# Kernel tuning notes

Measured on AMD Instinct MI355X. Metric: run time of the kernel, lower is better.

## Reference

```python
import jax, jax.numpy as jnp
import numpy as np

B, SIZE_IN, SIZE_OUT = 64, 1024, 1024


def setup_inputs() -> dict:
    key = jax.random.key(0)
    ks = jax.random.split(key, 6)
    mu_in = jax.random.normal(ks[0], (B, SIZE_IN), jnp.float32)
    # PSD input covariance: low-rank + jitter (sigma_in is a covariance matrix)
    L = jax.random.normal(ks[1], (B, SIZE_IN, 16), jnp.float32)
    sigma_in = jnp.einsum('bik,bjk->bij', L, L) / 16.0 + 1e-3 * jnp.eye(SIZE_IN, dtype=jnp.float32)
    bound = (1.0 / SIZE_IN) ** 0.5
    w_mu = jax.random.uniform(ks[2], (SIZE_IN, SIZE_OUT), jnp.float32, -bound, bound)
    b_mu = jax.random.uniform(ks[3], (SIZE_OUT, 1), jnp.float32, -bound, bound)
    w_sigma = jax.random.uniform(ks[4], (SIZE_OUT, SIZE_IN), jnp.float32, -12.0, -2.0)
    b_sigma = jax.random.uniform(ks[5], (SIZE_OUT,), jnp.float32, -12.0, -2.0)
    return {"mu_in": mu_in, "sigma_in": sigma_in, "w_mu": w_mu,
            "w_sigma": w_sigma, "b_mu": b_mu, "b_sigma": b_sigma}


def reference(mu_in, sigma_in, w_mu, w_sigma, b_mu, b_sigma):
    Bsz, n = mu_in.shape            # n = size_in
    m = w_mu.shape[1]               # m = size_out
    # mean propagation: (B, m, 1)
    mu_out = jnp.einsum('io,bi->bo', w_mu, mu_in)[:, :, None] + b_mu
    # diagonal weight/bias variances (softplus + epsilon), kept as vectors
    W_Sig = jax.nn.softplus(w_sigma) + 1e-6   # (m, n) == diag of diag_embed(W_Sigma)[o]
    B_Sig = jax.nn.softplus(b_sigma) + 1e-6   # (m,)
    # mu_in^T diag(W_Sig[o]) mu_in  -> (B, m)
    quad = jnp.einsum('oi,bi->bo', W_Sig, mu_in * mu_in)
    # faithful replication of torch's .view-based "trace" term:
    # W_Sigma.view(m, n*n) @ sigma_in.view(n*n, B), then result.view(B, m).
    # diag_embed rows only hit flat indices i*(n+1), so gather those rows.
    sig_flat = sigma_in.reshape(n * n, Bsz)            # memory reinterpret, like torch .view
    diag_rows = sig_flat[jnp.arange(n) * (n + 1)]      # (n, B)
    trW = (W_Sig @ diag_rows).reshape(Bsz, m)          # memory reinterpret, like torch .view
    # w_mu^T sigma_in w_mu : (B, m, m) -- dominant GEMM
    muT_sig_mu = jnp.einsum('io,bij,jp->bop', w_mu, sigma_in, w_mu)
    diag_term = trW + quad + B_Sig[None, :]            # (B, m)
    Sigma_out = muT_sig_mu + diag_term[:, :, None] * jnp.eye(m, dtype=mu_in.dtype)
    # KL vs standard normal; slogdet of a positive diagonal matrix == sum(log(diag))
    w_kl = 0.5 * jnp.sum(jnp.sum(W_Sig, axis=1) + jnp.sum(w_mu * w_mu, axis=0)
                         - n - jnp.sum(jnp.log(W_Sig), axis=1))
    b_kl = 0.5 * (jnp.sum(B_Sig) + jnp.sum(b_mu * b_mu) - m - jnp.sum(jnp.log(B_Sig)))
    return (mu_out, Sigma_out, w_kl, b_kl)
```

## Files before the change

### kernel.cpp

```cpp
#include <hip/hip_runtime.h>
#include <hip/hip_bf16.h>


typedef short bf16x8 __attribute__((ext_vector_type(8)));
typedef float f32x4  __attribute__((ext_vector_type(4)));
typedef unsigned short u16x8 __attribute__((ext_vector_type(8)));

__device__ __forceinline__ unsigned short f2bf(float f) {
    union { float f; unsigned u; } a; a.f = f;
    unsigned u = a.u;
    u += 0x7fffu + ((u >> 16) & 1u);
    return (unsigned short)(u >> 16);
}

__device__ __forceinline__ float softplus_eps(float x) {
    return fmaxf(x, 0.f) + log1pf(expf(-fabsf(x))) + 1e-6f;
}

__device__ __forceinline__ void gload_lds16(const unsigned short* g, unsigned short* l) {
    __builtin_amdgcn_global_load_lds(
        (const __attribute__((address_space(1))) void*)g,
        (__attribute__((address_space(3))) void*)l, 16, 0, 0);
}


__global__ void k_zero(float* acc) {
    if (threadIdx.x < 16) acc[threadIdx.x] = 0.f;
}

__global__ void k_convert(const float* __restrict__ src, unsigned short* __restrict__ dst) {
    const size_t i = ((size_t)blockIdx.x * 256 + threadIdx.x) * 8;
    const float4 a = *(const float4*)(src + i);
    const float4 b = *(const float4*)(src + i + 4);
    u16x8 h;
    h[0] = f2bf(a.x); h[1] = f2bf(a.y); h[2] = f2bf(a.z); h[3] = f2bf(a.w);
    h[4] = f2bf(b.x); h[5] = f2bf(b.y); h[6] = f2bf(b.z); h[7] = f2bf(b.w);
    *(u16x8*)(dst + i) = h;
}

__global__ void k_transpose(const float* __restrict__ wmu, float* __restrict__ wT32,
                            unsigned short* __restrict__ wTb, float* __restrict__ acc) {
    __shared__ float tile[64][65];
    const int bx = blockIdx.x;
    const int by = blockIdx.y;
    const int t = threadIdx.x;
    const int r = t >> 4;
    const int c4 = (t & 15) * 4;
    float s = 0.f;
#pragma unroll
    for (int p = 0; p < 4; ++p) {
        const int row = r + p * 16;
        const float4 v = *(const float4*)(wmu + (size_t)(bx * 64 + row) * 1024 + by * 64 + c4);
        tile[row][c4 + 0] = v.x; tile[row][c4 + 1] = v.y;
        tile[row][c4 + 2] = v.z; tile[row][c4 + 3] = v.w;
        s += v.x * v.x + v.y * v.y + v.z * v.z + v.w * v.w;
    }
    __syncthreads();
#pragma unroll
    for (int p = 0; p < 4; ++p) {
        const int row = r + p * 16;
        float4 o;
        o.x = tile[c4 + 0][row]; o.y = tile[c4 + 1][row];
        o.z = tile[c4 + 2][row]; o.w = tile[c4 + 3][row];
        const size_t off = (size_t)(by * 64 + row) * 1024 + bx * 64 + c4;
        *(float4*)(wT32 + off) = o;
        ushort4 h; h.x = f2bf(o.x); h.y = f2bf(o.y); h.z = f2bf(o.z); h.w = f2bf(o.w);
        *(ushort4*)(wTb + off) = h;
    }
#pragma unroll
    for (int off = 32; off; off >>= 1) s += __shfl_down(s, off, 64);
    if ((t & 63) == 0) atomicAdd(acc + 1, s);
}

__global__ void k_wsig(const float* __restrict__ wsg, float* __restrict__ WSig,
                       float* __restrict__ acc) {
    const int idx = (blockIdx.x * 256 + threadIdx.x) * 4;
    const float4 x = *(const float4*)(wsg + idx);
    float4 w;
    w.x = softplus_eps(x.x); w.y = softplus_eps(x.y);
    w.z = softplus_eps(x.z); w.w = softplus_eps(x.w);
    *(float4*)(WSig + idx) = w;
    float sw = w.x + w.y + w.z + w.w;
    float sl = logf(w.x) + logf(w.y) + logf(w.z) + logf(w.w);
#pragma unroll
    for (int off = 32; off; off >>= 1) {
        sw += __shfl_down(sw, off, 64);
        sl += __shfl_down(sl, off, 64);
    }
    if ((threadIdx.x & 63) == 0) { atomicAdd(acc + 0, sw); atomicAdd(acc + 2, sl); }
}

__global__ void k_gather(const float* __restrict__ sig, float* __restrict__ dr) {
    const int tg = blockIdx.x * 256 + threadIdx.x;
    const int k = tg >> 6, q = tg & 63;
    dr[tg] = sig[(size_t)k * 65600 + q];
}

__global__ void k_small(const float* __restrict__ mu_in, const float* __restrict__ wT32,
                        const float* __restrict__ WSig, const float* __restrict__ dr,
                        const float* __restrict__ b_mu, const float* __restrict__ b_sig,
                        float* __restrict__ mu_out, float* __restrict__ dterm) {
    __shared__ float mu_s[1024];
    __shared__ float m2_s[1024];
    const int blk = blockIdx.x;
    const int b = blk >> 2;
    const int o0 = (blk & 3) * 256;
    const int t = threadIdx.x;
    const int o = o0 + t;
    for (int j = t; j < 1024; j += 256) {
        const float v = mu_in[b * 1024 + j];
        mu_s[j] = v; m2_s[j] = v * v;
    }
    __syncthreads();
    const int rowTr = b * 16 + (o >> 6);
    const int qq = o & 63;
    const float* wrow = wT32 + (size_t)o * 1024;
    const float* srow = WSig + (size_t)o * 1024;
    const float* trow = WSig + (size_t)rowTr * 1024;
    float am = 0.f, aq = 0.f, at = 0.f;
#pragma unroll 4
    for (int i = 0; i < 1024; i += 4) {
        const float4 wv = *(const float4*)(wrow + i);
        const float4 sv = *(const float4*)(srow + i);
        const float4 tv = *(const float4*)(trow + i);
        const float4 mv = *(const float4*)(&mu_s[i]);
        const float4 m2 = *(const float4*)(&m2_s[i]);
        am += wv.x * mv.x + wv.y * mv.y + wv.z * mv.z + wv.w * mv.w;
        aq += sv.x * m2.x + sv.y * m2.y + sv.z * m2.z + sv.w * m2.w;
        at += tv.x * dr[(i + 0) * 64 + qq] + tv.y * dr[(i + 1) * 64 + qq]
            + tv.z * dr[(i + 2) * 64 + qq] + tv.w * dr[(i + 3) * 64 + qq];
    }
    const float bs = softplus_eps(b_sig[o]);
    dterm[b * 1024 + o] = at + aq + bs;
    mu_out[b * 1024 + o] = am + b_mu[o];
}

__global__ void k_final(const float* __restrict__ b_mu, const float* __restrict__ b_sig,
                        const float* __restrict__ acc, float* __restrict__ out) {
    __shared__ float red[3][4];
    const int t = threadIdx.x, lane = t & 63, w = t >> 6;
    float s1 = 0.f, s2 = 0.f, s3 = 0.f;
    for (int i = t; i < 1024; i += 256) {
        const float sp = softplus_eps(b_sig[i]);
        s1 += sp; s2 += logf(sp);
        const float bm = b_mu[i]; s3 += bm * bm;
    }
#pragma unroll
    for (int off = 32; off; off >>= 1) {
        s1 += __shfl_down(s1, off, 64);
        s2 += __shfl_down(s2, off, 64);
        s3 += __shfl_down(s3, off, 64);
    }
    if (lane == 0) { red[0][w] = s1; red[1][w] = s2; red[2][w] = s3; }
    __syncthreads();
    if (t == 0) {
        const float S1 = red[0][0] + red[0][1] + red[0][2] + red[0][3];
        const float S2 = red[1][0] + red[1][1] + red[1][2] + red[1][3];
        const float S3 = red[2][0] + red[2][1] + red[2][2] + red[2][3];
        out[67174401] = 0.5f * (S1 + S3 - 1024.f - S2);
        out[67174400] = 0.5f * (acc[0] + acc[1] - 1048576.f - acc[2]);
    }
}


__device__ __forceinline__ void stage_tile(const unsigned short* __restrict__ gsrc,
                                           unsigned short* ldst, int t, int k0) {
    const int tr = t >> 3;
    const int swz = (((t & 7) ^ (tr & 7)) << 3);
#pragma unroll
    for (int pass = 0; pass < 4; ++pass) {
        const int row = pass * 64 + tr;
        gload_lds16(gsrc + (size_t)row * 1024 + k0 + swz, ldst + pass * 4096 + t * 8);
    }
}

__device__ __forceinline__ void compute_tile(const unsigned short* Al, const unsigned short* Bl,
                                             f32x4 (&acc)[8][4], int wm, int wn, int q, int r) {
    const int swz = (r & 7) << 3;
#pragma unroll
    for (int ks = 0; ks < 2; ++ks) {
        const int co = (ks * 32 + q * 8) ^ swz;
        bf16x8 af[8], bv[4];
#pragma unroll
        for (int tm = 0; tm < 8; ++tm)
            af[tm] = *(const bf16x8*)(&Al[(wm * 128 + tm * 16 + r) * 64 + co]);
#pragma unroll
        for (int tn = 0; tn < 4; ++tn)
            bv[tn] = *(const bf16x8*)(&Bl[(wn * 64 + tn * 16 + r) * 64 + co]);
        __builtin_amdgcn_s_setprio(1);
#pragma unroll
        for (int tm = 0; tm < 8; ++tm)
#pragma unroll
            for (int tn = 0; tn < 4; ++tn)
                acc[tm][tn] = __builtin_amdgcn_mfma_f32_16x16x32_bf16(
                    af[tm], bv[tn], acc[tm][tn], 0, 0, 0);
        __builtin_amdgcn_s_setprio(0);
    }
}

__device__ __forceinline__ void run_gemm(const unsigned short* __restrict__ Ab,
                                         const unsigned short* __restrict__ Bb,
                                         unsigned short* lds, f32x4 (&acc)[8][4], int t) {
    const int lane = t & 63;
    const int wid = t >> 6;
    const int wm = wid >> 2, wn = wid & 3;
    const int q = lane >> 4, r = lane & 15;
#pragma unroll
    for (int a = 0; a < 8; ++a)
#pragma unroll
        for (int b = 0; b < 4; ++b) acc[a][b] = (f32x4){0.f, 0.f, 0.f, 0.f};

    stage_tile(Ab, lds + 0,     t, 0);
    stage_tile(Bb, lds + 16384, t, 0);
    stage_tile(Ab, lds + 32768, t, 64);
    stage_tile(Bb, lds + 49152, t, 64);
    asm volatile("s_waitcnt vmcnt(8)" ::: "memory");
    asm volatile("s_barrier" ::: "memory");

    for (int kt = 0; kt < 16; ++kt) {
        unsigned short* buf = lds + (kt & 1) * 32768;
        compute_tile(buf, buf + 16384, acc, wm, wn, q, r);
        asm volatile("s_waitcnt lgkmcnt(0)" ::: "memory");
        __builtin_amdgcn_sched_barrier(0);
        asm volatile("s_barrier" ::: "memory");
        if (kt + 2 < 16) {
            stage_tile(Ab, buf, t, (kt + 2) * 64);
            stage_tile(Bb, buf + 16384, t, (kt + 2) * 64);
            asm volatile("s_waitcnt vmcnt(8)" ::: "memory");
        } else {
            asm volatile("s_waitcnt vmcnt(0)" ::: "memory");
        }
        asm volatile("s_barrier" ::: "memory");
    }
}

__global__ __launch_bounds__(512) void k_gemmA(const unsigned short* __restrict__ sigb,
                                               const unsigned short* __restrict__ wT,
                                               unsigned short* __restrict__ Tp) {
    extern __shared__ unsigned short lds[];
    const int it_ = blockIdx.x;
    const int pt_ = blockIdx.y;
    const int bz  = blockIdx.z;
    const int t = threadIdx.x;
    const unsigned short* Ab = sigb + ((size_t)bz << 20) + (size_t)(it_ * 256) * 1024;
    const unsigned short* Bb = wT + (size_t)(pt_ * 256) * 1024;
    f32x4 acc[8][4];
    run_gemm(Ab, Bb, lds, acc, t);

    const int lane = t & 63, wid = t >> 6;
    const int wm = wid >> 2, wn = wid & 3;
    const int q = lane >> 4, r = lane & 15;
    unsigned short* Tb = Tp + ((size_t)bz << 20);
#pragma unroll
    for (int tm = 0; tm < 8; ++tm)
#pragma unroll
        for (int tn = 0; tn < 4; ++tn) {
            const f32x4 v = acc[tm][tn];
            const int i_e = it_ * 256 + wm * 128 + tm * 16 + q * 4;
            const int p_e = pt_ * 256 + wn * 64 + tn * 16 + r;
            ushort4 h; h.x = f2bf(v[0]); h.y = f2bf(v[1]); h.z = f2bf(v[2]); h.w = f2bf(v[3]);
            *(ushort4*)(Tb + (size_t)p_e * 1024 + i_e) = h;
        }
}

__global__ __launch_bounds__(512) void k_gemmB(const unsigned short* __restrict__ wT,
                                               const unsigned short* __restrict__ Tp,
                                               const float* __restrict__ dterm,
                                               float* __restrict__ Cs) {
    extern __shared__ unsigned short lds[];
    int ot_ = 0, rem = blockIdx.x;
    while (rem >= 4 - ot_) { rem -= 4 - ot_; ++ot_; }
    const int pt_ = ot_ + rem;
    const int bz  = blockIdx.z;
    const int t = threadIdx.x;
    const unsigned short* Ab = wT + (size_t)(ot_ * 256) * 1024;
    const unsigned short* Bb = Tp + ((size_t)bz << 20) + (size_t)(pt_ * 256) * 1024;
    f32x4 acc[8][4];
    run_gemm(Ab, Bb, lds, acc, t);

    const int lane = t & 63, wid = t >> 6;
    const int wm = wid >> 2, wn = wid & 3;
    const int q = lane >> 4, r = lane & 15;
    float* Cb = Cs + ((size_t)bz << 20);
    if (ot_ == pt_) {
#pragma unroll
        for (int tm = 0; tm < 8; ++tm)
#pragma unroll
            for (int tn = 0; tn < 4; ++tn) {
                const f32x4 v = acc[tm][tn];
                const int o_b = ot_ * 256 + wm * 128 + tm * 16 + q * 4;
                const int p_e = pt_ * 256 + wn * 64 + tn * 16 + r;
#pragma unroll
                for (int j = 0; j < 4; ++j) {
                    const int o = o_b + j;
                    float x = v[j];
                    if (o == p_e) x += dterm[bz * 1024 + o];
                    Cb[(size_t)o * 1024 + p_e] = x;
                }
            }
    } else {
#pragma unroll
        for (int tm = 0; tm < 8; ++tm)
#pragma unroll
            for (int tn = 0; tn < 4; ++tn) {
                const f32x4 v = acc[tm][tn];
                const int o_b = ot_ * 256 + wm * 128 + tm * 16 + q * 4;
                const int p_e = pt_ * 256 + wn * 64 + tn * 16 + r;
#pragma unroll
                for (int j = 0; j < 4; ++j)
                    Cb[(size_t)(o_b + j) * 1024 + p_e] = v[j];
                *(float4*)(Cb + (size_t)p_e * 1024 + o_b) =
                    (float4){v[0], v[1], v[2], v[3]};
            }
    }
}


extern "C" void kernel_launch(void* const* d_in, const int* in_sizes, int n_in,
                              void* d_out, int out_size, void* d_ws, size_t ws_size,
                              hipStream_t stream) {
    (void)in_sizes; (void)n_in; (void)out_size; (void)ws_size;
    const float* mu_in = (const float*)d_in[0];
    const float* sigma = (const float*)d_in[1];
    const float* w_mu  = (const float*)d_in[2];
    const float* w_sig = (const float*)d_in[3];
    const float* b_mu  = (const float*)d_in[4];
    const float* b_sg  = (const float*)d_in[5];
    float* out = (float*)d_out;

    char* ws = (char*)d_ws;
    unsigned short* Tp   = (unsigned short*)(ws + 0x0);
    float*          wT32 = (float*)(ws + 0x8000000);
    float*          WSig = (float*)(ws + 0x8400000);
    unsigned short* wTb  = (unsigned short*)(ws + 0x8800000);
    float*          dr   = (float*)(ws + 0x8A00000);
    float*          dt   = (float*)(ws + 0x8A40000);
    float*          acc  = (float*)(ws + 0x8A80000);

    unsigned short* sigb = (unsigned short*)(out + 65536);

    static bool attr_set = false;
    if (!attr_set) {
        hipFuncSetAttribute((const void*)k_gemmA,
                            hipFuncAttributeMaxDynamicSharedMemorySize, 131072);
        hipFuncSetAttribute((const void*)k_gemmB,
                            hipFuncAttributeMaxDynamicSharedMemorySize, 131072);
        attr_set = true;
    }

    k_zero<<<1, 64, 0, stream>>>(acc);
    k_convert<<<32768, 256, 0, stream>>>(sigma, sigb);
    k_transpose<<<dim3(16, 16), 256, 0, stream>>>(w_mu, wT32, wTb, acc);
    k_wsig<<<1024, 256, 0, stream>>>(w_sig, WSig, acc);
    k_gather<<<256, 256, 0, stream>>>(sigma, dr);
    k_small<<<256, 256, 0, stream>>>(mu_in, wT32, WSig, dr, b_mu, b_sg, out, dt);
    k_final<<<1, 256, 0, stream>>>(b_mu, b_sg, acc, out);
    k_gemmA<<<dim3(4, 4, 64), 512, 131072, stream>>>(sigb, wTb, Tp);
    k_gemmB<<<dim3(10, 1, 64), 512, 131072, stream>>>(wTb, Tp, dt, out + 65536);
}
```

Baseline: 968.1 us.

## Use 4-stage K32 LDS ring in GEMM and fold diagonal gather into convert

The GEMM main loop changes from a double-buffered K=64 tile scheme with two barriers per iteration to a 4-deep ring of K=32 stages with one barrier per iteration. The next stage's loads are issued before compute, with an adjusted swizzle. This aims to hide global-to-LDS latency and cut synchronisation overhead. The separate gather kernel is removed, and the convert kernel writes the needed diagonal rows of sigma from registers it already loaded, saving a launch and a re-read. Smaller K tiles mean more loop iterations and less MFMA work per barrier.

```diff
diff --git a/kernel.cpp b/kernel.cpp
--- a/kernel.cpp
+++ b/kernel.cpp
@@ -28,14 +28,23 @@
     if (threadIdx.x < 16) acc[threadIdx.x] = 0.f;
 }
 
-__global__ void k_convert(const float* __restrict__ src, unsigned short* __restrict__ dst) {
-    const size_t i = ((size_t)blockIdx.x * 256 + threadIdx.x) * 8;
-    const float4 a = *(const float4*)(src + i);
-    const float4 b = *(const float4*)(src + i + 4);
+__global__ void k_convert(const float* __restrict__ src, unsigned short* __restrict__ dst,
+                          float* __restrict__ dr) {
+    const unsigned i = blockIdx.x * 256 + threadIdx.x;
+    const size_t e = (size_t)i * 8;
+    const float4 a = *(const float4*)(src + e);
+    const float4 b = *(const float4*)(src + e + 4);
     u16x8 h;
     h[0] = f2bf(a.x); h[1] = f2bf(a.y); h[2] = f2bf(a.z); h[3] = f2bf(a.w);
     h[4] = f2bf(b.x); h[5] = f2bf(b.y); h[6] = f2bf(b.z); h[7] = f2bf(b.w);
-    *(u16x8*)(dst + i) = h;
+    *(u16x8*)(dst + e) = h;
+    const unsigned f8 = i * 8u;
+    const unsigned k = f8 / 65600u;
+    const unsigned rem = f8 - k * 65600u;
+    if (rem < 64u) {
+        *(float4*)(dr + k * 64 + rem) = a;
+        *(float4*)(dr + k * 64 + rem + 4) = b;
+    }
 }
 
 __global__ void k_transpose(const float* __restrict__ wmu, float* __restrict__ wT32,
@@ -88,12 +97,6 @@
         sl += __shfl_down(sl, off, 64);
     }
     if ((threadIdx.x & 63) == 0) { atomicAdd(acc + 0, sw); atomicAdd(acc + 2, sl); }
-}
-
-__global__ void k_gather(const float* __restrict__ sig, float* __restrict__ dr) {
-    const int tg = blockIdx.x * 256 + threadIdx.x;
-    const int k = tg >> 6, q = tg & 63;
-    dr[tg] = sig[(size_t)k * 65600 + q];
 }
 
 __global__ void k_small(const float* __restrict__ mu_in, const float* __restrict__ wT32,
@@ -163,46 +166,45 @@
 }
 
 
-__device__ __forceinline__ void stage_tile(const unsigned short* __restrict__ gsrc,
-                                           unsigned short* ldst, int t, int k0) {
-    const int tr = t >> 3;
-    const int swz = (((t & 7) ^ (tr & 7)) << 3);
-#pragma unroll
-    for (int pass = 0; pass < 4; ++pass) {
-        const int row = pass * 64 + tr;
-        gload_lds16(gsrc + (size_t)row * 1024 + k0 + swz, ldst + pass * 4096 + t * 8);
-    }
-}
-
-__device__ __forceinline__ void compute_tile(const unsigned short* Al, const unsigned short* Bl,
-                                             f32x4 (&acc)[8][4], int wm, int wn, int q, int r) {
-    const int swz = (r & 7) << 3;
-#pragma unroll
-    for (int ks = 0; ks < 2; ++ks) {
-        const int co = (ks * 32 + q * 8) ^ swz;
-        bf16x8 af[8], bv[4];
-#pragma unroll
-        for (int tm = 0; tm < 8; ++tm)
-            af[tm] = *(const bf16x8*)(&Al[(wm * 128 + tm * 16 + r) * 64 + co]);
+__device__ __forceinline__ void stage_kt(const unsigned short* __restrict__ A,
+                                         const unsigned short* __restrict__ B,
+                                         unsigned short* lds, int t, int kt) {
+    unsigned short* buf = lds + (kt & 3) * 16384;
+    const int u = t >> 2;
+    const int swz = (((t & 3) ^ ((u >> 1) & 3)) << 3);
+    const size_t k0 = (size_t)kt * 32 + swz;
+    gload_lds16(A + (size_t)u * 1024 + k0,         buf + t * 8);
+    gload_lds16(A + (size_t)(u + 128) * 1024 + k0, buf + 4096 + t * 8);
+    gload_lds16(B + (size_t)u * 1024 + k0,         buf + 8192 + t * 8);
+    gload_lds16(B + (size_t)(u + 128) * 1024 + k0, buf + 12288 + t * 8);
+}
+
+__device__ __forceinline__ void compute_kt(const unsigned short* buf, f32x4 (&acc)[8][4],
+                                           int wm, int wn, int q, int r) {
+    const int co = (q ^ ((r >> 1) & 3)) * 8;
+    const unsigned short* Ab = buf + (wm * 128 + r) * 32 + co;
+    const unsigned short* Bb = buf + 8192 + (wn * 64 + r) * 32 + co;
+    bf16x8 af[8], bv[4];
+#pragma unroll
+    for (int tn = 0; tn < 4; ++tn)
+        bv[tn] = *(const bf16x8*)(Bb + tn * 512);
+#pragma unroll
+    for (int tm = 0; tm < 8; ++tm)
+        af[tm] = *(const bf16x8*)(Ab + tm * 512);
+    __builtin_amdgcn_s_setprio(1);
+#pragma unroll
+    for (int tm = 0; tm < 8; ++tm)
 #pragma unroll
         for (int tn = 0; tn < 4; ++tn)
-            bv[tn] = *(const bf16x8*)(&Bl[(wn * 64 + tn * 16 + r) * 64 + co]);
-        __builtin_amdgcn_s_setprio(1);
-#pragma unroll
-        for (int tm = 0; tm < 8; ++tm)
-#pragma unroll
-            for (int tn = 0; tn < 4; ++tn)
-                acc[tm][tn] = __builtin_amdgcn_mfma_f32_16x16x32_bf16(
-                    af[tm], bv[tn], acc[tm][tn], 0, 0, 0);
-        __builtin_amdgcn_s_setprio(0);
-    }
+            acc[tm][tn] = __builtin_amdgcn_mfma_f32_16x16x32_bf16(
+                af[tm], bv[tn], acc[tm][tn], 0, 0, 0);
+    __builtin_amdgcn_s_setprio(0);
 }
 
 __device__ __forceinline__ void run_gemm(const unsigned short* __restrict__ Ab,
                                          const unsigned short* __restrict__ Bb,
                                          unsigned short* lds, f32x4 (&acc)[8][4], int t) {
-    const int lane = t & 63;
-    const int wid = t >> 6;
+    const int lane = t & 63, wid = t >> 6;
     const int wm = wid >> 2, wn = wid & 3;
     const int q = lane >> 4, r = lane & 15;
 #pragma unroll
@@ -210,28 +212,25 @@
 #pragma unroll
         for (int b = 0; b < 4; ++b) acc[a][b] = (f32x4){0.f, 0.f, 0.f, 0.f};
 
-    stage_tile(Ab, lds + 0,     t, 0);
-    stage_tile(Bb, lds + 16384, t, 0);
-    stage_tile(Ab, lds + 32768, t, 64);
-    stage_tile(Bb, lds + 49152, t, 64);
+    stage_kt(Ab, Bb, lds, t, 0);
+    stage_kt(Ab, Bb, lds, t, 1);
+    stage_kt(Ab, Bb, lds, t, 2);
+
+    for (int kt = 0; kt < 29; ++kt) {
+        asm volatile("s_waitcnt vmcnt(8)" ::: "memory");
+        asm volatile("s_barrier" ::: "memory");
+        stage_kt(Ab, Bb, lds, t, kt + 3);
+        compute_kt(lds + (kt & 3) * 16384, acc, wm, wn, q, r);
+    }
     asm volatile("s_waitcnt vmcnt(8)" ::: "memory");
     asm volatile("s_barrier" ::: "memory");
-
-    for (int kt = 0; kt < 16; ++kt) {
-        unsigned short* buf = lds + (kt & 1) * 32768;
-        compute_tile(buf, buf + 16384, acc, wm, wn, q, r);
-        asm volatile("s_waitcnt lgkmcnt(0)" ::: "memory");
-        __builtin_amdgcn_sched_barrier(0);
-        asm volatile("s_barrier" ::: "memory");
-        if (kt + 2 < 16) {
-            stage_tile(Ab, buf, t, (kt + 2) * 64);
-            stage_tile(Bb, buf + 16384, t, (kt + 2) * 64);
-            asm volatile("s_waitcnt vmcnt(8)" ::: "memory");
-        } else {
-            asm volatile("s_waitcnt vmcnt(0)" ::: "memory");
-        }
-        asm volatile("s_barrier" ::: "memory");
-    }
+    compute_kt(lds + (29 & 3) * 16384, acc, wm, wn, q, r);
+    asm volatile("s_waitcnt vmcnt(4)" ::: "memory");
+    asm volatile("s_barrier" ::: "memory");
+    compute_kt(lds + (30 & 3) * 16384, acc, wm, wn, q, r);
+    asm volatile("s_waitcnt vmcnt(0)" ::: "memory");
+    asm volatile("s_barrier" ::: "memory");
+    compute_kt(lds + (31 & 3) * 16384, acc, wm, wn, q, r);
 }
 
 __global__ __launch_bounds__(512) void k_gemmA(const unsigned short* __restrict__ sigb,
@@ -349,10 +348,9 @@
     }
 
     k_zero<<<1, 64, 0, stream>>>(acc);
-    k_convert<<<32768, 256, 0, stream>>>(sigma, sigb);
+    k_convert<<<32768, 256, 0, stream>>>(sigma, sigb, dr);
     k_transpose<<<dim3(16, 16), 256, 0, stream>>>(w_mu, wT32, wTb, acc);
     k_wsig<<<1024, 256, 0, stream>>>(w_sig, WSig, acc);
-    k_gather<<<256, 256, 0, stream>>>(sigma, dr);
     k_small<<<256, 256, 0, stream>>>(mu_in, wT32, WSig, dr, b_mu, b_sg, out, dt);
     k_final<<<1, 256, 0, stream>>>(b_mu, b_sg, acc, out);
     k_gemmA<<<dim3(4, 4, 64), 512, 131072, stream>>>(sigb, wTb, Tp);
```

Result: faster. 939.7 us (-2.9%).
